# Kernel optimization log

Hardware: AMD Instinct MI355X
Metric: run time of the kernel (lower is better)

## Reference

```python
import jax, jax.numpy as jnp
import numpy as np

EPS = 1e-8


def setup_inputs() -> dict:
    key = jax.random.key(0)
    k1, k2 = jax.random.split(key)
    B, C, L = 16, 4, 4096
    K, S = 256, 128
    x = jax.random.normal(k1, (B, C, L), dtype=jnp.float32)
    shapelets = jax.random.normal(k2, (C, K, S), dtype=jnp.float32)
    return {"x": x, "shapelets": shapelets}


def reference(x, shapelets):
    # x: (B, C, L); shapelets: (C, K, S)
    B, C, L = x.shape
    _, K, S = shapelets.shape
    W = L - S + 1  # number of sliding windows

    # unfold: (B, C, W, S) sliding windows with stride 1
    idx = jnp.arange(W)[:, None] + jnp.arange(S)[None, :]  # (W, S)
    win = x[:, :, idx]  # (B, C, W, S)
    win = win / jnp.maximum(jnp.linalg.norm(win, axis=-1, keepdims=True), EPS)

    shp = shapelets / jnp.maximum(
        jnp.linalg.norm(shapelets, axis=-1, keepdims=True), EPS
    )  # (C, K, S)

    # pairwise dot products: (B, C, W, K)
    sim = jnp.einsum("bcws,cks->bcwk", win, shp)
    # sum over channels, keepdim, transpose(2,3), divide by n_dims
    sim = jnp.sum(sim, axis=1, keepdims=True) / C  # (B, 1, W, K)
    sim = jnp.transpose(sim, (0, 1, 3, 2))  # (B, 1, K, W)
    sim = jax.nn.relu(sim)
    # global max-pool over window positions -> (B, 1, K)
    return jnp.max(sim, axis=3)
```

## Files before the change

### kernel.cpp

```cpp
#include <hip/hip_runtime.h>
#include <hip/hip_bf16.h>

#define NB 16
#define NC 4
#define NL 4096
#define NK 256
#define NS 128
#define NW (NL - NS + 1)
#define WPB 256
#define KPB 128
#define XEL 384
#define XROW 400
#define EPSF 1e-8f

typedef __attribute__((ext_vector_type(8))) _Float16 f16x8;
typedef __attribute__((ext_vector_type(4))) float floatx4;

typedef __attribute__((address_space(3))) unsigned int* lds_ptr_t;
typedef const __attribute__((address_space(1))) unsigned int* gbl_ptr_t;

__device__ inline short f2h(float f) {
    _Float16 h = (_Float16)f;
    short s;
    __builtin_memcpy(&s, &h, sizeof(short));
    return s;
}

__device__ inline void gload_lds16(const void* g, void* l) {
    __builtin_amdgcn_global_load_lds((gbl_ptr_t)g, (lds_ptr_t)l, 16, 0, 0);
}

__global__ __launch_bounds__(64)
void norm_shp_kernel(const float* __restrict__ shp, short* __restrict__ shpn) {
    int ck = blockIdx.x;
    int k = ck & (NK - 1);
    int lane = threadIdx.x;
    const float* p = shp + (size_t)ck * NS;
    float v0 = p[lane];
    float v1 = p[lane + 64];
    float ss = v0 * v0 + v1 * v1;
    #pragma unroll
    for (int o = 32; o > 0; o >>= 1) ss += __shfl_xor(ss, o, 64);
    float rn = 1.f / fmaxf(sqrtf(ss), EPSF);
    int s0 = lane, s1 = lane + 64;
    int d0 = ((((s0 >> 3) ^ (k & 15)) << 3) | (s0 & 7));
    int d1 = ((((s1 >> 3) ^ (k & 15)) << 3) | (s1 & 7));
    shpn[(size_t)ck * NS + d0] = f2h(v0 * rn);
    shpn[(size_t)ck * NS + d1] = f2h(v1 * rn);
}

__global__ __launch_bounds__(512, 1)
void mcs_main_kernel(const float* __restrict__ x,
                     const short* __restrict__ shpn,
                     float* __restrict__ out) {
    __shared__ f16x8 bs[NC][KPB * 16];
    __shared__ alignas(16) short xcp[NC][4][XROW];
    __shared__ alignas(16) float scratch[NC][XEL];
    __shared__ float invw[NC][WPB];
    __shared__ float epi[8][64];

    const int kq = blockIdx.x, slot = blockIdx.y;
    const int b = slot >> 3, wslot = slot & 7;
    const int tid = threadIdx.x;
    const int lane = tid & 63, wv = tid >> 6;
    const int m = lane & 15, q = lane >> 4, r = m & 3;
    const int kh = wv & 1, wh = wv >> 1;

    {
        const char* gbase = (const char*)shpn + (size_t)(kq * KPB) * NS * 2;
        #pragma unroll
        for (int c = 0; c < NC; c++) {
            const char* gc = gbase + (size_t)c * NK * NS * 2;
            char* lc = (char*)&bs[c][0];
            #pragma unroll
            for (int i = 0; i < 4; i++) {
                int off = (wv * 4 + i) * 1024;
                gload_lds16(gc + off + lane * 16, lc + off);
            }
        }
    }

    float xv[8];
    #pragma unroll
    for (int t = 0; t < 2; t++) {
        const int g = (wslot * 2 + t) * WPB + tid;
        #pragma unroll
        for (int c = 0; c < NC; c++)
            xv[t * 4 + c] = (tid < XEL && g < NL)
                          ? x[((size_t)b * NC + c) * NL + g] : 0.f;
    }

    float res[2];

    #pragma unroll
    for (int t = 0; t < 2; t++) {
        const int w0 = (wslot * 2 + t) * WPB;

        if (tid < XEL) {
            #pragma unroll
            for (int c = 0; c < NC; c++) {
                float xf = xv[t * 4 + c];
                short hv = f2h(xf);
                #pragma unroll
                for (int rr = 0; rr < 4; rr++) {
                    int o2 = tid - rr;
                    if (o2 >= 0) xcp[c][rr][o2] = hv;
                }
                scratch[c][tid] = xf * xf;
            }
        }
        __syncthreads();

        if (wv < 4) {
            const int c = wv;
            const int base = lane * 6;
            float v[6];
            #pragma unroll
            for (int i = 0; i < 6; i++) v[i] = scratch[c][base + i];
            #pragma unroll
            for (int i = 1; i < 6; i++) v[i] += v[i - 1];
            float tt = v[5];
            #pragma unroll
            for (int o = 1; o < 64; o <<= 1) {
                float u = __shfl_up(tt, o, 64);
                if (lane >= o) tt += u;
            }
            float excl = tt - v[5];
            #pragma unroll
            for (int i = 0; i < 6; i++) scratch[c][base + i] = v[i] + excl;
        }
        __syncthreads();

        #pragma unroll
        for (int i = 0; i < 2; i++) {
            int ii = tid + 512 * i;
            int c = ii >> 8, o = ii & 255;
            float nn = scratch[c][o + 127] - (o ? scratch[c][o - 1] : 0.f);
            int w = w0 + o;
            invw[c][o] = (w < NW) ? 1.f / fmaxf(sqrtf(fmaxf(nn, 0.f)), EPSF)
                                  : 0.f;
        }
        if (t == 0) asm volatile("s_waitcnt vmcnt(0)" ::: "memory");
        __syncthreads();

        floatx4 tot[4][4];
        #pragma unroll
        for (int mt = 0; mt < 4; mt++)
            #pragma unroll
            for (int kt = 0; kt < 4; kt++)
                tot[mt][kt] = (floatx4){0.f, 0.f, 0.f, 0.f};

        #pragma unroll
        for (int c = 0; c < NC; c++) {
            f16x8 ivs[4];
            #pragma unroll
            for (int mt = 0; mt < 4; mt++) {
                _Float16 ih = (_Float16)invw[c][wh * 64 + mt * 16 + m];
                ivs[mt] = (f16x8){ih, ih, ih, ih, ih, ih, ih, ih};
            }
            #pragma unroll
            for (int s0 = 0; s0 < NS; s0 += 32) {
                f16x8 a[4];
                #pragma unroll
                for (int mt = 0; mt < 4; mt++) {
                    int ts = wh * 64 + mt * 16 + m + s0 + q * 8;
                    const uint2* pp = (const uint2*)&xcp[c][r][ts - r];
                    union { uint2 uu[2]; f16x8 v; } cv;
                    cv.uu[0] = pp[0]; cv.uu[1] = pp[1];
                    a[mt] = cv.v * ivs[mt];
                }
                int cc = (s0 >> 3) + q;
                #pragma unroll
                for (int kt = 0; kt < 4; kt++) {
                    int k = kh * 64 + kt * 16 + m;
                    f16x8 bf = bs[c][(k << 4) | (cc ^ m)];
                    #pragma unroll
                    for (int mt = 0; mt < 4; mt++)
                        tot[mt][kt] = __builtin_amdgcn_mfma_f32_16x16x32_f16(
                            a[mt], bf, tot[mt][kt], 0, 0, 0);
                }
            }
        }

        #pragma unroll
        for (int kt = 0; kt < 4; kt++) {
            floatx4 v0 = tot[0][kt], v1 = tot[1][kt],
                    v2 = tot[2][kt], v3 = tot[3][kt];
            float mx = fmaxf(fmaxf(fmaxf(v0.x, v0.y), fmaxf(v0.z, v0.w)),
                             fmaxf(fmaxf(v1.x, v1.y), fmaxf(v1.z, v1.w)));
            mx = fmaxf(mx, fmaxf(fmaxf(fmaxf(v2.x, v2.y), fmaxf(v2.z, v2.w)),
                                 fmaxf(fmaxf(v3.x, v3.y), fmaxf(v3.z, v3.w))));
            mx = fmaxf(mx, __shfl_xor(mx, 16, 64));
            mx = fmaxf(mx, __shfl_xor(mx, 32, 64));
            if (lane < 16) epi[wv][kt * 16 + lane] = mx;
        }
        __syncthreads();
        if (tid < 128) {
            int kh_ = tid >> 6, j = tid & 63;
            float v = fmaxf(fmaxf(epi[kh_][j],     epi[kh_ + 2][j]),
                            fmaxf(epi[kh_ + 4][j], epi[kh_ + 6][j]));
            res[t] = fmaxf(v, 0.f) * 0.25f;
        }
        __syncthreads();
    }

    if (tid < 128) {
        int kg = kq * KPB + tid;
        #pragma unroll
        for (int t = 0; t < 2; t++)
            atomicMax((int*)out + (size_t)b * NK + kg, __float_as_int(res[t]));
    }
}

extern "C" void kernel_launch(void* const* d_in, const int* in_sizes, int n_in,
                              void* d_out, int out_size, void* d_ws, size_t ws_size,
                              hipStream_t stream) {
    (void)in_sizes; (void)n_in; (void)out_size; (void)ws_size;
    const float* x   = (const float*)d_in[0];
    const float* shp = (const float*)d_in[1];
    float* out = (float*)d_out;

    short* shpn = (short*)d_ws;

    norm_shp_kernel<<<NC * NK, 64, 0, stream>>>(shp, shpn);
    mcs_main_kernel<<<dim3(2, 128), 512, 0, stream>>>(x, shpn, out);
}
```

Before: 71.97 us.

## Process 512 windows per block in one pass with 8 M-tiles per wave

```diff
diff --git a/kernel.cpp b/kernel.cpp
--- a/kernel.cpp
+++ b/kernel.cpp
@@ -7,13 +7,14 @@
 #define NK 256
 #define NS 128
 #define NW (NL - NS + 1)
-#define WPB 256
+#define WPB 512
 #define KPB 128
-#define XEL 384
-#define XROW 400
+#define XEL 640
+#define XROW 656
 #define EPSF 1e-8f
 
 typedef __attribute__((ext_vector_type(8))) _Float16 f16x8;
+typedef __attribute__((ext_vector_type(2))) _Float16 f16x2;
 typedef __attribute__((ext_vector_type(4))) float floatx4;
 
 typedef __attribute__((address_space(3))) unsigned int* lds_ptr_t;
@@ -55,12 +56,14 @@
                      float* __restrict__ out) {
     __shared__ f16x8 bs[NC][KPB * 16];
     __shared__ alignas(16) short xcp[NC][4][XROW];
-    __shared__ alignas(16) float scratch[NC][XEL];
-    __shared__ float invw[NC][WPB];
-    __shared__ float epi[8][64];
+    __shared__ union {
+        float scratch[NC][XEL];
+        struct { float invw[NC][WPB]; float epi[8][64]; } c;
+    } u;
 
     const int kq = blockIdx.x, slot = blockIdx.y;
     const int b = slot >> 3, wslot = slot & 7;
+    const int w0 = wslot * WPB;
     const int tid = threadIdx.x;
     const int lane = tid & 63, wv = tid >> 6;
     const int m = lane & 15, q = lane >> 4, r = m & 3;
@@ -80,135 +83,138 @@
         }
     }
 
-    float xv[8];
-    #pragma unroll
-    for (int t = 0; t < 2; t++) {
-        const int g = (wslot * 2 + t) * WPB + tid;
+    float xv[NC], xv2[NC];
+    {
+        const int g0 = w0 + tid;
         #pragma unroll
         for (int c = 0; c < NC; c++)
-            xv[t * 4 + c] = (tid < XEL && g < NL)
-                          ? x[((size_t)b * NC + c) * NL + g] : 0.f;
-    }
-
-    float res[2];
-
-    #pragma unroll
-    for (int t = 0; t < 2; t++) {
-        const int w0 = (wslot * 2 + t) * WPB;
-
-        if (tid < XEL) {
-            #pragma unroll
-            for (int c = 0; c < NC; c++) {
-                float xf = xv[t * 4 + c];
-                short hv = f2h(xf);
+            xv[c] = (g0 < NL) ? x[((size_t)b * NC + c) * NL + g0] : 0.f;
+        if (tid < XEL - 512) {
+            const int g1 = g0 + 512;
+            #pragma unroll
+            for (int c = 0; c < NC; c++)
+                xv2[c] = (g1 < NL) ? x[((size_t)b * NC + c) * NL + g1] : 0.f;
+        }
+    }
+
+    #pragma unroll
+    for (int c = 0; c < NC; c++) {
+        short hv = f2h(xv[c]);
+        #pragma unroll
+        for (int rr = 0; rr < 4; rr++) {
+            int o2 = tid - rr;
+            if (o2 >= 0) xcp[c][rr][o2] = hv;
+        }
+        u.scratch[c][tid] = xv[c] * xv[c];
+        if (tid < XEL - 512) {
+            short hv2 = f2h(xv2[c]);
+            #pragma unroll
+            for (int rr = 0; rr < 4; rr++)
+                xcp[c][rr][tid + 512 - rr] = hv2;
+            u.scratch[c][tid + 512] = xv2[c] * xv2[c];
+        }
+    }
+    __syncthreads();
+
+    if (wv < 4) {
+        const int c = wv;
+        const int base = lane * 10;
+        float v[10];
+        #pragma unroll
+        for (int i = 0; i < 10; i++) v[i] = u.scratch[c][base + i];
+        #pragma unroll
+        for (int i = 1; i < 10; i++) v[i] += v[i - 1];
+        float tt = v[9];
+        #pragma unroll
+        for (int o = 1; o < 64; o <<= 1) {
+            float uu = __shfl_up(tt, o, 64);
+            if (lane >= o) tt += uu;
+        }
+        float excl = tt - v[9];
+        #pragma unroll
+        for (int i = 0; i < 10; i++) u.scratch[c][base + i] = v[i] + excl;
+    }
+    __syncthreads();
+
+    float ivreg[4];
+    #pragma unroll
+    for (int i = 0; i < 4; i++) {
+        int ii = tid + 512 * i;
+        int c = ii >> 9, o = ii & 511;
+        float nn = u.scratch[c][o + 127] - (o ? u.scratch[c][o - 1] : 0.f);
+        int w = w0 + o;
+        ivreg[i] = (w < NW) ? 1.f / fmaxf(sqrtf(fmaxf(nn, 0.f)), EPSF) : 0.f;
+    }
+    __syncthreads();
+    #pragma unroll
+    for (int i = 0; i < 4; i++) {
+        int ii = tid + 512 * i;
+        u.c.invw[ii >> 9][ii & 511] = ivreg[i];
+    }
+    asm volatile("s_waitcnt vmcnt(0)" ::: "memory");
+    __syncthreads();
+
+    floatx4 tot[8][4];
+    #pragma unroll
+    for (int mt = 0; mt < 8; mt++)
+        #pragma unroll
+        for (int kt = 0; kt < 4; kt++)
+            tot[mt][kt] = (floatx4){0.f, 0.f, 0.f, 0.f};
+
+    #pragma unroll
+    for (int c = 0; c < NC; c++) {
+        f16x2 iv2[8];
+        #pragma unroll
+        for (int mt = 0; mt < 8; mt++) {
+            _Float16 ih = (_Float16)u.c.invw[c][wh * 128 + mt * 16 + m];
+            iv2[mt] = (f16x2){ih, ih};
+        }
+        #pragma unroll
+        for (int s0 = 0; s0 < NS; s0 += 32) {
+            f16x8 a[8];
+            #pragma unroll
+            for (int mt = 0; mt < 8; mt++) {
+                int ts = wh * 128 + mt * 16 + m + s0 + q * 8;
+                const uint2* pp = (const uint2*)&xcp[c][r][ts - r];
+                union { uint2 uu[2]; f16x8 v; f16x2 h2[4]; } cv;
+                cv.uu[0] = pp[0]; cv.uu[1] = pp[1];
                 #pragma unroll
-                for (int rr = 0; rr < 4; rr++) {
-                    int o2 = tid - rr;
-                    if (o2 >= 0) xcp[c][rr][o2] = hv;
-                }
-                scratch[c][tid] = xf * xf;
+                for (int p2 = 0; p2 < 4; p2++) cv.h2[p2] *= iv2[mt];
+                a[mt] = cv.v;
             }
-        }
-        __syncthreads();
-
-        if (wv < 4) {
-            const int c = wv;
-            const int base = lane * 6;
-            float v[6];
-            #pragma unroll
-            for (int i = 0; i < 6; i++) v[i] = scratch[c][base + i];
-            #pragma unroll
-            for (int i = 1; i < 6; i++) v[i] += v[i - 1];
-            float tt = v[5];
-            #pragma unroll
-            for (int o = 1; o < 64; o <<= 1) {
-                float u = __shfl_up(tt, o, 64);
-                if (lane >= o) tt += u;
+            int cc = (s0 >> 3) + q;
+            #pragma unroll
+            for (int kt = 0; kt < 4; kt++) {
+                int k = kh * 64 + kt * 16 + m;
+                f16x8 bf = bs[c][(k << 4) | (cc ^ m)];
+                #pragma unroll
+                for (int mt = 0; mt < 8; mt++)
+                    tot[mt][kt] = __builtin_amdgcn_mfma_f32_16x16x32_f16(
+                        a[mt], bf, tot[mt][kt], 0, 0, 0);
             }
-            float excl = tt - v[5];
-            #pragma unroll
-            for (int i = 0; i < 6; i++) scratch[c][base + i] = v[i] + excl;
-        }
-        __syncthreads();
-
-        #pragma unroll
-        for (int i = 0; i < 2; i++) {
-            int ii = tid + 512 * i;
-            int c = ii >> 8, o = ii & 255;
-            float nn = scratch[c][o + 127] - (o ? scratch[c][o - 1] : 0.f);
-            int w = w0 + o;
-            invw[c][o] = (w < NW) ? 1.f / fmaxf(sqrtf(fmaxf(nn, 0.f)), EPSF)
-                                  : 0.f;
-        }
-        if (t == 0) asm volatile("s_waitcnt vmcnt(0)" ::: "memory");
-        __syncthreads();
-
-        floatx4 tot[4][4];
-        #pragma unroll
-        for (int mt = 0; mt < 4; mt++)
-            #pragma unroll
-            for (int kt = 0; kt < 4; kt++)
-                tot[mt][kt] = (floatx4){0.f, 0.f, 0.f, 0.f};
-
-        #pragma unroll
-        for (int c = 0; c < NC; c++) {
-            f16x8 ivs[4];
-            #pragma unroll
-            for (int mt = 0; mt < 4; mt++) {
-                _Float16 ih = (_Float16)invw[c][wh * 64 + mt * 16 + m];
-                ivs[mt] = (f16x8){ih, ih, ih, ih, ih, ih, ih, ih};
-            }
-            #pragma unroll
-            for (int s0 = 0; s0 < NS; s0 += 32) {
-                f16x8 a[4];
-                #pragma unroll
-                for (int mt = 0; mt < 4; mt++) {
-                    int ts = wh * 64 + mt * 16 + m + s0 + q * 8;
-                    const uint2* pp = (const uint2*)&xcp[c][r][ts - r];
-                    union { uint2 uu[2]; f16x8 v; } cv;
-                    cv.uu[0] = pp[0]; cv.uu[1] = pp[1];
-                    a[mt] = cv.v * ivs[mt];
-                }
-                int cc = (s0 >> 3) + q;
-                #pragma unroll
-                for (int kt = 0; kt < 4; kt++) {
-                    int k = kh * 64 + kt * 16 + m;
-                    f16x8 bf = bs[c][(k << 4) | (cc ^ m)];
-                    #pragma unroll
-                    for (int mt = 0; mt < 4; mt++)
-                        tot[mt][kt] = __builtin_amdgcn_mfma_f32_16x16x32_f16(
-                            a[mt], bf, tot[mt][kt], 0, 0, 0);
-                }
-            }
-        }
-
-        #pragma unroll
-        for (int kt = 0; kt < 4; kt++) {
-            floatx4 v0 = tot[0][kt], v1 = tot[1][kt],
-                    v2 = tot[2][kt], v3 = tot[3][kt];
-            float mx = fmaxf(fmaxf(fmaxf(v0.x, v0.y), fmaxf(v0.z, v0.w)),
-                             fmaxf(fmaxf(v1.x, v1.y), fmaxf(v1.z, v1.w)));
-            mx = fmaxf(mx, fmaxf(fmaxf(fmaxf(v2.x, v2.y), fmaxf(v2.z, v2.w)),
-                                 fmaxf(fmaxf(v3.x, v3.y), fmaxf(v3.z, v3.w))));
-            mx = fmaxf(mx, __shfl_xor(mx, 16, 64));
-            mx = fmaxf(mx, __shfl_xor(mx, 32, 64));
-            if (lane < 16) epi[wv][kt * 16 + lane] = mx;
-        }
-        __syncthreads();
-        if (tid < 128) {
-            int kh_ = tid >> 6, j = tid & 63;
-            float v = fmaxf(fmaxf(epi[kh_][j],     epi[kh_ + 2][j]),
-                            fmaxf(epi[kh_ + 4][j], epi[kh_ + 6][j]));
-            res[t] = fmaxf(v, 0.f) * 0.25f;
-        }
-        __syncthreads();
-    }
-
+        }
+    }
+
+    #pragma unroll
+    for (int kt = 0; kt < 4; kt++) {
+        float mx = -1e30f;
+        #pragma unroll
+        for (int mt = 0; mt < 8; mt++) {
+            floatx4 v = tot[mt][kt];
+            mx = fmaxf(mx, fmaxf(fmaxf(v.x, v.y), fmaxf(v.z, v.w)));
+        }
+        mx = fmaxf(mx, __shfl_xor(mx, 16, 64));
+        mx = fmaxf(mx, __shfl_xor(mx, 32, 64));
+        if (lane < 16) u.c.epi[wv][kt * 16 + lane] = mx;
+    }
+    __syncthreads();
     if (tid < 128) {
-        int kg = kq * KPB + tid;
-        #pragma unroll
-        for (int t = 0; t < 2; t++)
-            atomicMax((int*)out + (size_t)b * NK + kg, __float_as_int(res[t]));
+        int kh_ = tid >> 6, j = tid & 63;
+        float v = fmaxf(fmaxf(u.c.epi[kh_][j],     u.c.epi[kh_ + 2][j]),
+                        fmaxf(u.c.epi[kh_ + 4][j], u.c.epi[kh_ + 6][j]));
+        v = fmaxf(v, 0.f) * 0.25f;
+        atomicMax((int*)out + (size_t)b * NK + kq * KPB + tid,
+                  __float_as_int(v));
     }
 }
 
```

New measurement: 70.25 us (median of 2 runs). -2.4%, faster.
